# Kernel optimization log

Measured on AMD Instinct MI355X. Metric: run time of the kernel, lower is better.

Reference implementation:

```python
import jax, jax.numpy as jnp
import numpy as np

B, I, J, DIN, DOUT = 256, 1152, 10, 8, 16
ROUTING_ITERS = 3


def squash(v):
    # v: [..., D]; squash(v) = (|v|^2 / (1+|v|^2)) * v/|v| = v * |v| / (1+|v|^2)
    l2 = jnp.linalg.norm(v, axis=-1, keepdims=True)
    return v * (l2 / (1.0 + l2 * l2))


def setup_inputs() -> dict:
    key = jax.random.key(0)
    k1, k2 = jax.random.split(key)
    x = jax.random.normal(k1, (B, I, DIN), dtype=jnp.float32)
    # per-(i,j) Linear(DIN -> DOUT, bias=False) weights, stacked: [I, J, DOUT, DIN]
    W = jax.random.normal(k2, (I, J, DOUT, DIN), dtype=jnp.float32) * 0.1
    return {"x": x, "W": W}


def reference(x, W):
    # prediction vectors u[b,i,j,:] = W[i,j] @ x[b,i,:]  -> [B, I, J, DOUT]
    u = jnp.einsum('bid,ijod->bijo', x, W)
    b = jnp.zeros((I, J), dtype=u.dtype)  # routing logits (shared across batch)
    s = None
    for _ in range(ROUTING_ITERS):
        c = jax.nn.softmax(b, axis=-1)              # [I, J]
        s = jnp.einsum('ij,bijd->bjd', c, u)        # coupling-weighted sum over in-caps
        s = squash(s)                               # [B, J, DOUT]
        # agreement: b[i,j] += sum_b <u[b,i,j], s[b,j]>
        b = b + jnp.einsum('bijd,bjd->ij', u, s)
    return s
```

## Files before the change

kernel.cpp:

```cpp
#include <hip/hip_runtime.h>
#include <math.h>

typedef unsigned short ushort_t;
typedef __attribute__((ext_vector_type(8))) __bf16 bf16x8;
typedef __attribute__((ext_vector_type(4))) float floatx4;

#define B_    256
#define I_    1152
#define J_    10
#define DIN_  8
#define DOUT_ 16
#define K_    (I_*DIN_)
#define N_    (J_*DOUT_)
#define WPS   16
#define KCHUNK (K_/WPS)
#define KSTEPS (KCHUNK/32)

static __device__ __forceinline__ ushort_t f2bf(float f) {
    unsigned int u = __float_as_uint(f);
    u += 0x7fffu + ((u >> 16) & 1u);
    return (ushort_t)(u >> 16);
}
static __device__ __forceinline__ float bf2f(ushort_t h) {
    return __uint_as_float(((unsigned int)h) << 16);
}

__global__ __launch_bounds__(1024)
void gemm_s_fused_kernel(const float* __restrict__ x, const float* __restrict__ W,
                         const float* __restrict__ blog, float* __restrict__ s_out,
                         ushort_t* __restrict__ Sbt_hi, ushort_t* __restrict__ Sbt_lo,
                         ushort_t* __restrict__ Wc_hi, ushort_t* __restrict__ Wc_lo,
                         const int iter)
{
    const int tid  = threadIdx.x;
    const int tile = blockIdx.x;
    const int lane = tid & 63;
    const int w    = tid >> 6;
    const int mb   = tile / J_;
    const int nt   = tile - mb * J_;

    __shared__ float  c_lds[I_];
    __shared__ floatx4 part[WPS * 64];

    if (iter > 0) {
        for (int r2 = tid; r2 < I_; r2 += 1024) {
            const float* br = blog + (size_t)r2 * J_;
            float bv[J_];
            float mx = -1e30f;
            #pragma unroll
            for (int j = 0; j < J_; ++j) { bv[j] = br[j]; mx = fmaxf(mx, bv[j]); }
            float sum = 0.f;
            #pragma unroll
            for (int j = 0; j < J_; ++j) { bv[j] = __expf(bv[j] - mx); sum += bv[j]; }
            c_lds[r2] = bv[nt] / sum;
        }
        __syncthreads();
    }

    {
        const int r = lane & 15, q = lane >> 4;
        const float* ap = x + (size_t)(mb * 16 + r) * K_ + w * KCHUNK + 8 * q;
        const size_t wei = (((size_t)(w * 72 + q) * J_ + nt) * DOUT_ + r) * DIN_;
        const size_t wstep = (size_t)4 * J_ * DOUT_ * DIN_;
        floatx4 acc = {0.f, 0.f, 0.f, 0.f};

        if (iter == 0) {
            #pragma unroll
            for (int s = 0; s < KSTEPS; ++s) {
                float4 xa0 = *(const float4*)(ap + s * 32);
                float4 xa1 = *(const float4*)(ap + s * 32 + 4);
                float4 w0  = *(const float4*)(W + wei + s * wstep);
                float4 w1  = *(const float4*)(W + wei + s * wstep + 4);
                float xv[8]  = {xa0.x, xa0.y, xa0.z, xa0.w, xa1.x, xa1.y, xa1.z, xa1.w};
                float wvv[8] = {w0.x, w0.y, w0.z, w0.w, w1.x, w1.y, w1.z, w1.w};
                bf16x8 ah, al, bh, bl;
                #pragma unroll
                for (int e = 0; e < 8; ++e) {
                    float xe = xv[e] * 0.1f;
                    __bf16 h = (__bf16)xe;
                    ah[e] = h;
                    al[e] = (__bf16)(xe - (float)h);
                    float pe = wvv[e];
                    __bf16 g = (__bf16)pe;
                    bh[e] = g;
                    bl[e] = (__bf16)(pe - (float)g);
                }
                *(bf16x8*)(Wc_hi + wei + s * wstep) = bh;
                *(bf16x8*)(Wc_lo + wei + s * wstep) = bl;
                acc = __builtin_amdgcn_mfma_f32_16x16x32_bf16(ah, bh, acc, 0, 0, 0);
                acc = __builtin_amdgcn_mfma_f32_16x16x32_bf16(al, bh, acc, 0, 0, 0);
                acc = __builtin_amdgcn_mfma_f32_16x16x32_bf16(ah, bl, acc, 0, 0, 0);
            }
        } else {
            #pragma unroll
            for (int s = 0; s < KSTEPS; ++s) {
                float4 xa0 = *(const float4*)(ap + s * 32);
                float4 xa1 = *(const float4*)(ap + s * 32 + 4);
                bf16x8 bh = *(const bf16x8*)(Wc_hi + wei + s * wstep);
                bf16x8 bl = *(const bf16x8*)(Wc_lo + wei + s * wstep);
                float cs  = c_lds[w * 72 + 4 * s + q];
                float xv[8] = {xa0.x, xa0.y, xa0.z, xa0.w, xa1.x, xa1.y, xa1.z, xa1.w};
                bf16x8 ah, al;
                #pragma unroll
                for (int e = 0; e < 8; ++e) {
                    float xe = xv[e] * cs;
                    __bf16 h = (__bf16)xe;
                    ah[e] = h;
                    al[e] = (__bf16)(xe - (float)h);
                }
                acc = __builtin_amdgcn_mfma_f32_16x16x32_bf16(ah, bh, acc, 0, 0, 0);
                acc = __builtin_amdgcn_mfma_f32_16x16x32_bf16(al, bh, acc, 0, 0, 0);
                acc = __builtin_amdgcn_mfma_f32_16x16x32_bf16(ah, bl, acc, 0, 0, 0);
            }
        }
        part[w * 64 + lane] = acc;
    }
    __syncthreads();

    if (tid < 256) {
        const int b_local = tid >> 4;
        const int o       = tid & 15;
        const int lane_c  = ((b_local >> 2) << 4) | o;
        const int reg     = b_local & 3;
        float v = 0.f;
        #pragma unroll
        for (int u = 0; u < WPS; ++u)
            v += part[u * 64 + lane_c][reg];
        float sq = v * v;
        #pragma unroll
        for (int off = 1; off < 16; off <<= 1)
            sq += __shfl_xor(sq, off, 16);
        float l2 = sqrtf(sq);
        float val = v * (l2 / (1.f + sq));
        const int b  = mb * 16 + b_local;
        const int jo = nt * 16 + o;
        if (iter == 2) {
            s_out[(size_t)b * N_ + jo] = val;
        } else {
            ushort_t hi = f2bf(val);
            Sbt_hi[(size_t)jo * B_ + b] = hi;
            Sbt_lo[(size_t)jo * B_ + b] = f2bf(val - bf2f(hi));
        }
    }
}

__global__ __launch_bounds__(256)
void gemm_bupd_kernel(const float* __restrict__ x,
                      const ushort_t* __restrict__ Sbt_hi, const ushort_t* __restrict__ Sbt_lo,
                      const float* __restrict__ W, float* __restrict__ blog,
                      const int first)
{
    int wv   = blockIdx.x * 4 + (threadIdx.x >> 6);
    int lane = threadIdx.x & 63;
    int mt = wv / 5;
    int jp = wv - mt * 5;
    int j0 = jp * 2, j1 = jp * 2 + 1;
    int r = lane & 15, q = lane >> 4;
    const float* xp = x + (size_t)(8 * q) * K_ + (mt * 16 + r);
    size_t b0off = (size_t)(j0 * 16 + r) * B_ + 8 * q;
    size_t b1off = (size_t)(j1 * 16 + r) * B_ + 8 * q;
    floatx4 acc0 = {0.f, 0.f, 0.f, 0.f};
    floatx4 acc1 = {0.f, 0.f, 0.f, 0.f};
    #pragma unroll
    for (int s = 0; s < B_ / 32; ++s) {
        bf16x8 ah, al;
        #pragma unroll
        for (int e = 0; e < 8; ++e) {
            float v = xp[(size_t)(s * 32 + e) * K_];
            __bf16 h = (__bf16)v;
            ah[e] = h;
            al[e] = (__bf16)(v - (float)h);
        }
        bf16x8 bh0 = *(const bf16x8*)(Sbt_hi + b0off + s * 32);
        bf16x8 bl0 = *(const bf16x8*)(Sbt_lo + b0off + s * 32);
        bf16x8 bh1 = *(const bf16x8*)(Sbt_hi + b1off + s * 32);
        bf16x8 bl1 = *(const bf16x8*)(Sbt_lo + b1off + s * 32);
        acc0 = __builtin_amdgcn_mfma_f32_16x16x32_bf16(ah, bh0, acc0, 0, 0, 0);
        acc0 = __builtin_amdgcn_mfma_f32_16x16x32_bf16(al, bh0, acc0, 0, 0, 0);
        acc0 = __builtin_amdgcn_mfma_f32_16x16x32_bf16(ah, bl0, acc0, 0, 0, 0);
        acc1 = __builtin_amdgcn_mfma_f32_16x16x32_bf16(ah, bh1, acc1, 0, 0, 0);
        acc1 = __builtin_amdgcn_mfma_f32_16x16x32_bf16(al, bh1, acc1, 0, 0, 0);
        acc1 = __builtin_amdgcn_mfma_f32_16x16x32_bf16(ah, bl1, acc1, 0, 0, 0);
    }
    int i  = mt * 2 + (q >> 1);
    int d0 = (q & 1) * 4;
    int o  = lane & 15;
    int iw = mt * 2 + (lane >> 5);
    {
        const float4 w4 = *(const float4*)(W + ((((size_t)i * J_ + j0) * DOUT_ + o) * DIN_ + d0));
        float val = acc0[0] * w4.x + acc0[1] * w4.y + acc0[2] * w4.z + acc0[3] * w4.w;
        #pragma unroll
        for (int off = 1; off < 32; off <<= 1)
            val += __shfl_xor(val, off, 32);
        if ((lane & 31) == 0) {
            float* dst = blog + (size_t)iw * J_ + j0;
            if (first) *dst = val; else *dst += val;
        }
    }
    {
        const float4 w4 = *(const float4*)(W + ((((size_t)i * J_ + j1) * DOUT_ + o) * DIN_ + d0));
        float val = acc1[0] * w4.x + acc1[1] * w4.y + acc1[2] * w4.z + acc1[3] * w4.w;
        #pragma unroll
        for (int off = 1; off < 32; off <<= 1)
            val += __shfl_xor(val, off, 32);
        if ((lane & 31) == 0) {
            float* dst = blog + (size_t)iw * J_ + j1;
            if (first) *dst = val; else *dst += val;
        }
    }
}

extern "C" void kernel_launch(void* const* d_in, const int* in_sizes, int n_in,
                              void* d_out, int out_size, void* d_ws, size_t ws_size,
                              hipStream_t stream)
{
    const float* x = (const float*)d_in[0];
    const float* W = (const float*)d_in[1];
    float* s_out = (float*)d_out;

    char* ws = (char*)d_ws;
    ushort_t* Sbt_hi = (ushort_t*)(ws);
    ushort_t* Sbt_lo = (ushort_t*)(ws + 81920);
    float*    blog   = (float*)   (ws + 163840);
    ushort_t* Wc_hi  = (ushort_t*)(ws + 209920);
    ushort_t* Wc_lo  = (ushort_t*)(ws + 3159040);

    for (int it = 0; it < 3; ++it) {
        gemm_s_fused_kernel<<<160, 1024, 0, stream>>>(x, W, blog, s_out,
                                                      Sbt_hi, Sbt_lo,
                                                      Wc_hi, Wc_lo, it);
        if (it < 2)
            gemm_bupd_kernel<<<720, 256, 0, stream>>>(x, Sbt_hi, Sbt_lo,
                                                      W, blog, it == 0 ? 1 : 0);
    }
}
```

Before: 168.1 us.

## Drop cached bf16 W split, remap blocks across XCDs, prefetch next K-step loads

Removes the Wc_hi/Wc_lo workspace that cached the bf16 hi/lo split of W. Every iteration now re-reads fp32 W and splits it on the fly, with the coupling coefficient folded into W instead of x. Block indices are remapped so tiles sharing the same x rows or W column land on the same XCD, aiming for better L2 reuse. Both GEMM loops add register double-buffering of the next step's global loads. The trade is extra conversion ALU work and higher fp32 W traffic in later iterations, in exchange for no bf16 writes in iteration 0 and better latency hiding.

```diff
diff --git a/kernel.cpp b/kernel.cpp
--- a/kernel.cpp
+++ b/kernel.cpp
@@ -29,17 +29,18 @@
 void gemm_s_fused_kernel(const float* __restrict__ x, const float* __restrict__ W,
                          const float* __restrict__ blog, float* __restrict__ s_out,
                          ushort_t* __restrict__ Sbt_hi, ushort_t* __restrict__ Sbt_lo,
-                         ushort_t* __restrict__ Wc_hi, ushort_t* __restrict__ Wc_lo,
                          const int iter)
 {
     const int tid  = threadIdx.x;
-    const int tile = blockIdx.x;
+    const int blk  = blockIdx.x;
+    const int xcd  = blk & 7;
+    const int sl   = blk >> 3;
+    const int mb   = (xcd >> 1) * 4 + (sl & 3);
+    const int nt   = (xcd & 1) * 5 + (sl >> 2);
     const int lane = tid & 63;
     const int w    = tid >> 6;
-    const int mb   = tile / J_;
-    const int nt   = tile - mb * J_;
-
-    __shared__ float  c_lds[I_];
+
+    __shared__ float   c_lds[I_];
     __shared__ floatx4 part[WPS * 64];
 
     if (iter > 0) {
@@ -60,58 +61,42 @@
     {
         const int r = lane & 15, q = lane >> 4;
         const float* ap = x + (size_t)(mb * 16 + r) * K_ + w * KCHUNK + 8 * q;
-        const size_t wei = (((size_t)(w * 72 + q) * J_ + nt) * DOUT_ + r) * DIN_;
+        const float* wp = W + (((size_t)(w * 72 + q) * J_ + nt) * DOUT_ + r) * DIN_;
         const size_t wstep = (size_t)4 * J_ * DOUT_ * DIN_;
         floatx4 acc = {0.f, 0.f, 0.f, 0.f};
 
-        if (iter == 0) {
-            #pragma unroll
-            for (int s = 0; s < KSTEPS; ++s) {
-                float4 xa0 = *(const float4*)(ap + s * 32);
-                float4 xa1 = *(const float4*)(ap + s * 32 + 4);
-                float4 w0  = *(const float4*)(W + wei + s * wstep);
-                float4 w1  = *(const float4*)(W + wei + s * wstep + 4);
-                float xv[8]  = {xa0.x, xa0.y, xa0.z, xa0.w, xa1.x, xa1.y, xa1.z, xa1.w};
-                float wvv[8] = {w0.x, w0.y, w0.z, w0.w, w1.x, w1.y, w1.z, w1.w};
-                bf16x8 ah, al, bh, bl;
-                #pragma unroll
-                for (int e = 0; e < 8; ++e) {
-                    float xe = xv[e] * 0.1f;
-                    __bf16 h = (__bf16)xe;
-                    ah[e] = h;
-                    al[e] = (__bf16)(xe - (float)h);
-                    float pe = wvv[e];
-                    __bf16 g = (__bf16)pe;
-                    bh[e] = g;
-                    bl[e] = (__bf16)(pe - (float)g);
-                }
-                *(bf16x8*)(Wc_hi + wei + s * wstep) = bh;
-                *(bf16x8*)(Wc_lo + wei + s * wstep) = bl;
-                acc = __builtin_amdgcn_mfma_f32_16x16x32_bf16(ah, bh, acc, 0, 0, 0);
-                acc = __builtin_amdgcn_mfma_f32_16x16x32_bf16(al, bh, acc, 0, 0, 0);
-                acc = __builtin_amdgcn_mfma_f32_16x16x32_bf16(ah, bl, acc, 0, 0, 0);
+        float4 xa0 = *(const float4*)(ap);
+        float4 xa1 = *(const float4*)(ap + 4);
+        float4 w0  = *(const float4*)(wp);
+        float4 w1  = *(const float4*)(wp + 4);
+        #pragma unroll
+        for (int s = 0; s < KSTEPS; ++s) {
+            float4 nxa0, nxa1, nw0, nw1;
+            if (s + 1 < KSTEPS) {
+                nxa0 = *(const float4*)(ap + (s + 1) * 32);
+                nxa1 = *(const float4*)(ap + (s + 1) * 32 + 4);
+                nw0  = *(const float4*)(wp + (s + 1) * wstep);
+                nw1  = *(const float4*)(wp + (s + 1) * wstep + 4);
             }
-        } else {
-            #pragma unroll
-            for (int s = 0; s < KSTEPS; ++s) {
-                float4 xa0 = *(const float4*)(ap + s * 32);
-                float4 xa1 = *(const float4*)(ap + s * 32 + 4);
-                bf16x8 bh = *(const bf16x8*)(Wc_hi + wei + s * wstep);
-                bf16x8 bl = *(const bf16x8*)(Wc_lo + wei + s * wstep);
-                float cs  = c_lds[w * 72 + 4 * s + q];
-                float xv[8] = {xa0.x, xa0.y, xa0.z, xa0.w, xa1.x, xa1.y, xa1.z, xa1.w};
-                bf16x8 ah, al;
-                #pragma unroll
-                for (int e = 0; e < 8; ++e) {
-                    float xe = xv[e] * cs;
-                    __bf16 h = (__bf16)xe;
-                    ah[e] = h;
-                    al[e] = (__bf16)(xe - (float)h);
-                }
-                acc = __builtin_amdgcn_mfma_f32_16x16x32_bf16(ah, bh, acc, 0, 0, 0);
-                acc = __builtin_amdgcn_mfma_f32_16x16x32_bf16(al, bh, acc, 0, 0, 0);
-                acc = __builtin_amdgcn_mfma_f32_16x16x32_bf16(ah, bl, acc, 0, 0, 0);
+            float cs   = (iter == 0) ? 0.1f : c_lds[w * 72 + 4 * s + q];
+            float xv[8]  = {xa0.x, xa0.y, xa0.z, xa0.w, xa1.x, xa1.y, xa1.z, xa1.w};
+            float wvv[8] = {w0.x, w0.y, w0.z, w0.w, w1.x, w1.y, w1.z, w1.w};
+            bf16x8 ah, al, bh, bl;
+            #pragma unroll
+            for (int e = 0; e < 8; ++e) {
+                float xe = xv[e];
+                __bf16 h = (__bf16)xe;
+                ah[e] = h;
+                al[e] = (__bf16)(xe - (float)h);
+                float pe = wvv[e] * cs;
+                __bf16 g = (__bf16)pe;
+                bh[e] = g;
+                bl[e] = (__bf16)(pe - (float)g);
             }
+            acc = __builtin_amdgcn_mfma_f32_16x16x32_bf16(ah, bh, acc, 0, 0, 0);
+            acc = __builtin_amdgcn_mfma_f32_16x16x32_bf16(al, bh, acc, 0, 0, 0);
+            acc = __builtin_amdgcn_mfma_f32_16x16x32_bf16(ah, bl, acc, 0, 0, 0);
+            if (s + 1 < KSTEPS) { xa0 = nxa0; xa1 = nxa1; w0 = nw0; w1 = nw1; }
         }
         part[w * 64 + lane] = acc;
     }
@@ -161,12 +146,21 @@
     size_t b1off = (size_t)(j1 * 16 + r) * B_ + 8 * q;
     floatx4 acc0 = {0.f, 0.f, 0.f, 0.f};
     floatx4 acc1 = {0.f, 0.f, 0.f, 0.f};
+
+    float xcur[8], xnxt[8];
+    #pragma unroll
+    for (int e = 0; e < 8; ++e) xcur[e] = xp[(size_t)e * K_];
     #pragma unroll
     for (int s = 0; s < B_ / 32; ++s) {
+        if (s + 1 < B_ / 32) {
+            #pragma unroll
+            for (int e = 0; e < 8; ++e)
+                xnxt[e] = xp[(size_t)((s + 1) * 32 + e) * K_];
+        }
         bf16x8 ah, al;
         #pragma unroll
         for (int e = 0; e < 8; ++e) {
-            float v = xp[(size_t)(s * 32 + e) * K_];
+            float v = xcur[e];
             __bf16 h = (__bf16)v;
             ah[e] = h;
             al[e] = (__bf16)(v - (float)h);
@@ -181,6 +175,8 @@
         acc1 = __builtin_amdgcn_mfma_f32_16x16x32_bf16(ah, bh1, acc1, 0, 0, 0);
         acc1 = __builtin_amdgcn_mfma_f32_16x16x32_bf16(al, bh1, acc1, 0, 0, 0);
         acc1 = __builtin_amdgcn_mfma_f32_16x16x32_bf16(ah, bl1, acc1, 0, 0, 0);
+        #pragma unroll
+        for (int e = 0; e < 8; ++e) xcur[e] = xnxt[e];
     }
     int i  = mt * 2 + (q >> 1);
     int d0 = (q & 1) * 4;
@@ -222,13 +218,10 @@
     ushort_t* Sbt_hi = (ushort_t*)(ws);
     ushort_t* Sbt_lo = (ushort_t*)(ws + 81920);
     float*    blog   = (float*)   (ws + 163840);
-    ushort_t* Wc_hi  = (ushort_t*)(ws + 209920);
-    ushort_t* Wc_lo  = (ushort_t*)(ws + 3159040);
 
     for (int it = 0; it < 3; ++it) {
         gemm_s_fused_kernel<<<160, 1024, 0, stream>>>(x, W, blog, s_out,
-                                                      Sbt_hi, Sbt_lo,
-                                                      Wc_hi, Wc_lo, it);
+                                                      Sbt_hi, Sbt_lo, it);
         if (it < 2)
             gemm_bupd_kernel<<<720, 256, 0, stream>>>(x, Sbt_hi, Sbt_lo,
                                                       W, blog, it == 0 ? 1 : 0);
```

Result: faster. 160.6 us (-4.5%).
